# Optimization experiments

Measured on AMD Instinct MI355X. Metric: run time of the kernel, lower is better.

Reference implementation:

```python
import jax, jax.numpy as jnp
import numpy as np

SEQ = 2048
DIM = 512
HEADS = 8
DH = DIM // HEADS
EPS = float(np.finfo(np.float32).eps)
NEG = float(np.finfo(np.float32).max)


def _pos_encoding(seq, dim):
    idx = jnp.arange(seq, dtype=jnp.float32)
    div = 1.0 / (10000.0 ** (jnp.arange(0, dim, 2, dtype=jnp.float32) / dim) + EPS)
    ang = idx[:, None] * div[None, :]  # [S, dim/2]
    pos = jnp.zeros((seq, dim), dtype=jnp.float32)
    pos = pos.at[:, 0::2].set(jnp.sin(ang)).at[:, 1::2].set(jnp.cos(ang))
    return pos[None]  # [1, S, D]


def _rmsnorm(x, gain, bias):
    d = x.shape[-1]
    scale = jnp.linalg.norm(x, axis=-1, keepdims=True) * (d ** -0.5)
    return x / (scale + EPS) * gain + bias


def setup_inputs() -> dict:
    key = jax.random.key(0)
    ks = jax.random.split(key, 12)
    s = 0.02
    return {
        "x": jax.random.normal(ks[0], (4, SEQ, DIM), dtype=jnp.float32),
        "norm1_g": jnp.ones((DIM,), jnp.float32),
        "norm1_b": jnp.zeros((DIM,), jnp.float32),
        "wq": jax.random.normal(ks[1], (DIM, DIM), jnp.float32) * s,
        "wk": jax.random.normal(ks[2], (DIM, DIM), jnp.float32) * s,
        "wv": jax.random.normal(ks[3], (DIM, DIM), jnp.float32) * s,
        "wo": jax.random.normal(ks[4], (DIM, DIM), jnp.float32) * s,
        "norm2_g": jnp.ones((DIM,), jnp.float32),
        "norm2_b": jnp.zeros((DIM,), jnp.float32),
        "ff_w1": jax.random.normal(ks[5], (DIM, DIM), jnp.float32) * s,
        "ff_b1": jnp.zeros((DIM,), jnp.float32),
        "ffn_g": jnp.ones((DIM,), jnp.float32),
        "ffn_b": jnp.zeros((DIM,), jnp.float32),
        "sw_w": jax.random.normal(ks[6], (2 * DIM, DIM), jnp.float32) * s,
        "sw_b": jnp.zeros((2 * DIM,), jnp.float32),
        "ff_w2": jax.random.normal(ks[7], (DIM, DIM), jnp.float32) * s,
        "ff_b2": jnp.zeros((DIM,), jnp.float32),
    }


def _block(x, norm1_g, norm1_b, wq, wk, wv, wo, norm2_g, norm2_b,
           ff_w1, ff_b1, ffn_g, ffn_b, sw_w, sw_b, ff_w2, ff_b2):
    B = x.shape[0]
    x = x + _pos_encoding(SEQ, DIM)

    # --- multi-head attention on RMSNorm(x) ---
    h = _rmsnorm(x, norm1_g, norm1_b)
    q = (h @ wq.T).reshape(B, SEQ, HEADS, DH).transpose(0, 2, 1, 3)  # [B,H,S,Dh]
    k = (h @ wk.T).reshape(B, SEQ, HEADS, DH).transpose(0, 2, 1, 3)
    v = (h @ wv.T).reshape(B, SEQ, HEADS, DH).transpose(0, 2, 1, 3)
    scores = jnp.einsum("bhqd,bhkd->bhqk", q, k)  # materialized [B,H,S,S]
    causal_mask = jnp.triu(jnp.ones((SEQ, SEQ), dtype=bool), k=1)
    scores = jnp.where(causal_mask[None, None], -NEG, scores)
    # NOTE: original scales by dim_k**-0.5 = dim_emb**-0.5 (not head dim)
    attn = jax.nn.softmax(scores * (DIM ** -0.5), axis=-1)
    o = jnp.einsum("bhqk,bhkd->bhqd", attn, v)
    o = o.transpose(0, 2, 1, 3).reshape(B, SEQ, DIM) @ wo.T
    x = x + o

    # --- feed-forward: Linear -> RMSNorm -> SwiGLU -> Linear ---
    h = _rmsnorm(x, norm2_g, norm2_b)
    h = h @ ff_w1.T + ff_b1
    h = _rmsnorm(h, ffn_g, ffn_b)
    u = h @ sw_w.T + sw_b  # [B,S,2*DIM]
    h = jax.nn.silu(u[..., :DIM]) + u[..., DIM:]
    h = h @ ff_w2.T + ff_b2
    return x + h


def reference(x, norm1_g, norm1_b, wq, wk, wv, wo, norm2_g, norm2_b,
              ff_w1, ff_b1, ffn_g, ffn_b, sw_w, sw_b, ff_w2, ff_b2):
    return _block(x, norm1_g, norm1_b, wq, wk, wv, wo, norm2_g, norm2_b,
                  ff_w1, ff_b1, ffn_g, ffn_b, sw_w, sw_b, ff_w2, ff_b2)
```

## Files before the change

### kernel.cpp

```cpp
#include <hip/hip_runtime.h>
#include <hip/hip_bf16.h>
#include <cstdint>
#include <cstddef>

typedef __bf16 bf16;
typedef __bf16 bf16x4_t __attribute__((ext_vector_type(4)));
typedef __bf16 bf16x8_t __attribute__((ext_vector_type(8)));
typedef float f32x4 __attribute__((ext_vector_type(4)));
typedef float f32x16 __attribute__((ext_vector_type(16)));

#define DEV_INLINE __device__ __forceinline__

constexpr int SEQ = 2048, DIM = 512, HEADS = 8, DH = 64;
constexpr int ROWS = 4 * SEQ;
constexpr float EPSF = 1.1920928955078125e-07f;
constexpr float RSQRT_DIM = 0.04419417382415922f;
constexpr float LOG2E = 1.44269504088896f;

DEV_INLINE void load_lds16(const void* g, void* l) {
  __builtin_amdgcn_global_load_lds(
      (const __attribute__((address_space(1))) void*)g,
      (__attribute__((address_space(3))) void*)l,
      16, 0, 0);
}

DEV_INLINE unsigned int packbf(float a, float b) {
  union { unsigned int u; bf16 h[2]; } z;
  z.h[0] = (bf16)a;
  z.h[1] = (bf16)b;
  return z.u;
}

DEV_INLINE void permswap(unsigned int& a, unsigned int& b) {
  asm volatile("v_permlane32_swap_b32 %0, %1" : "+v"(a), "+v"(b));
}

__global__ __launch_bounds__(256) void cvt_all_k(
    const float* __restrict__ wq, const float* __restrict__ wk,
    const float* __restrict__ wv, const float* __restrict__ wo,
    const float* __restrict__ w1, const float* __restrict__ sww,
    const float* __restrict__ w2, bf16* __restrict__ dst) {
  const int i = blockIdx.x * 256 + threadIdx.x;
  const float* src;
  int local;
  if (i < 196608)      { src = (i < 65536) ? wq : (i < 131072) ? wk : wv; local = i & 65535; }
  else if (i < 262144) { src = wo;  local = i - 196608; }
  else if (i < 327680) { src = w1;  local = i - 262144; }
  else if (i < 458752) { src = sww; local = i - 327680; }
  else                 { src = w2;  local = i - 458752; }
  float4 f = reinterpret_cast<const float4*>(src)[local];
  bf16x4_t o;
  o[0] = (bf16)f.x; o[1] = (bf16)f.y; o[2] = (bf16)f.z; o[3] = (bf16)f.w;
  reinterpret_cast<bf16x4_t*>(dst)[i] = o;
}

template <bool ADDPOS>
__global__ __launch_bounds__(256) void rmsnorm_k(const float* __restrict__ in,
                                                 const float* __restrict__ gain,
                                                 const float* __restrict__ bias,
                                                 float* __restrict__ outF,
                                                 bf16* __restrict__ outB) {
  const int sub = threadIdx.x >> 7;
  const int row = blockIdx.x * 2 + sub;
  const int t = threadIdx.x & 127;
  const float* rp = in + (size_t)row * DIM;
  float4 v = reinterpret_cast<const float4*>(rp)[t];
  if constexpr (ADDPOS) {
    const int s = row & (SEQ - 1);
    const float e0 = (float)(4 * t) * (1.0f / (float)DIM);
    const float e1 = (float)(4 * t + 2) * (1.0f / (float)DIM);
    const float d0 = 1.0f / (powf(10000.0f, e0) + EPSF);
    const float d1 = 1.0f / (powf(10000.0f, e1) + EPSF);
    const float a0 = (float)s * d0, a1 = (float)s * d1;
    v.x += sinf(a0); v.y += cosf(a0);
    v.z += sinf(a1); v.w += cosf(a1);
  }
  float ss = v.x * v.x + v.y * v.y + v.z * v.z + v.w * v.w;
#pragma unroll
  for (int off = 32; off > 0; off >>= 1) ss += __shfl_down(ss, off, 64);
  __shared__ float red[4];
  const int wv = threadIdx.x >> 6;
  if ((threadIdx.x & 63) == 0) red[wv] = ss;
  __syncthreads();
  const float total = red[sub * 2] + red[sub * 2 + 1];
  const float scale = sqrtf(total) * RSQRT_DIM;
  const float inv = 1.0f / (scale + EPSF);
  if constexpr (ADDPOS)
    reinterpret_cast<float4*>(outF + (size_t)row * DIM)[t] = v;
  const float4 g = reinterpret_cast<const float4*>(gain)[t];
  const float4 bb = reinterpret_cast<const float4*>(bias)[t];
  bf16x4_t o;
  o[0] = (bf16)(v.x * inv * g.x + bb.x);
  o[1] = (bf16)(v.y * inv * g.y + bb.y);
  o[2] = (bf16)(v.z * inv * g.z + bb.z);
  o[3] = (bf16)(v.w * inv * g.w + bb.w);
  reinterpret_cast<bf16x4_t*>(outB + (size_t)row * DIM)[t] = o;
}

enum { MODE_QKV = 0, MODE_RES = 1, MODE_BIAS = 2, MODE_SWIGLU2 = 3, MODE_RESBIAS = 4 };

template <int MODE>
__global__ __launch_bounds__(256) void gemm_bt_k(
    const bf16* __restrict__ A, const bf16* __restrict__ Bt,
    const float* __restrict__ bias, const float* __restrict__ res,
    float* __restrict__ outF, bf16* __restrict__ outB,
    bf16* __restrict__ oq, bf16* __restrict__ okk, bf16* __restrict__ ovT) {
  constexpr int BELEMS = (MODE == MODE_SWIGLU2) ? 4096 : 2048;
  __shared__ __align__(16) bf16 sA[4][128 * 32];
  __shared__ __align__(16) bf16 sB[4][BELEMS];
  const int tid = threadIdx.x;
  const int wave = tid >> 6, lane = tid & 63;
  const int m0 = blockIdx.x * 128, n0 = blockIdx.y * 64;
  const int wm = wave >> 1, wn = wave & 1;
  const int lr = lane & 15, lk = (lane >> 4) * 8;

  const f32x4 fzero = {0.f, 0.f, 0.f, 0.f};
  f32x4 acc[4][2], acc2[4][2];
#pragma unroll
  for (int i = 0; i < 4; ++i)
#pragma unroll
    for (int j = 0; j < 2; ++j) { acc[i][j] = fzero; acc2[i][j] = fzero; }

  const int off0 = wave * 1024 + lane * 16;
  const int rowS = off0 >> 6, colb = off0 & 63;

  auto stage = [&](int buf, int kt) {
    const int k0 = kt * 32;
    load_lds16((const char*)A + ((size_t)(m0 + rowS) * 512 + k0) * 2 + colb,
               (char*)&sA[buf][0] + off0);
    load_lds16((const char*)A + ((size_t)(m0 + 64 + rowS) * 512 + k0) * 2 + colb,
               (char*)&sA[buf][0] + 4096 + off0);
    load_lds16((const char*)Bt + ((size_t)(n0 + rowS) * 512 + k0) * 2 + colb,
               (char*)&sB[buf][0] + off0);
    if constexpr (MODE == MODE_SWIGLU2)
      load_lds16((const char*)Bt + ((size_t)(512 + n0 + rowS) * 512 + k0) * 2 + colb,
                 (char*)&sB[buf][0] + 4096 + off0);
  };

  stage(0, 0);
  stage(1, 1);
  stage(2, 2);
  if constexpr (MODE == MODE_SWIGLU2)
    asm volatile("s_waitcnt vmcnt(8)\ns_barrier" ::: "memory");
  else
    asm volatile("s_waitcnt vmcnt(6)\ns_barrier" ::: "memory");

#pragma unroll
  for (int kt = 0; kt < 16; ++kt) {
    const int cur = kt & 3;
    if (kt + 3 < 16) stage((kt + 3) & 3, kt + 3);
    bf16x8_t af[4], bfr[2], bfr2[2];
#pragma unroll
    for (int mf = 0; mf < 4; ++mf)
      af[mf] = *(const bf16x8_t*)(&sA[cur][0] + (wm * 64 + mf * 16 + lr) * 32 + lk);
#pragma unroll
    for (int nf = 0; nf < 2; ++nf)
      bfr[nf] = *(const bf16x8_t*)(&sB[cur][0] + (wn * 32 + nf * 16 + lr) * 32 + lk);
    if constexpr (MODE == MODE_SWIGLU2) {
#pragma unroll
      for (int nf = 0; nf < 2; ++nf)
        bfr2[nf] = *(const bf16x8_t*)(&sB[cur][0] + 2048 + (wn * 32 + nf * 16 + lr) * 32 + lk);
    }
    asm volatile("s_waitcnt lgkmcnt(0)" ::: "memory");
#pragma unroll
    for (int mf = 0; mf < 4; ++mf)
#pragma unroll
      for (int nf = 0; nf < 2; ++nf) {
        acc[mf][nf] = __builtin_amdgcn_mfma_f32_16x16x32_bf16(af[mf], bfr[nf],
                                                              acc[mf][nf], 0, 0, 0);
        if constexpr (MODE == MODE_SWIGLU2)
          acc2[mf][nf] = __builtin_amdgcn_mfma_f32_16x16x32_bf16(af[mf], bfr2[nf],
                                                                 acc2[mf][nf], 0, 0, 0);
      }
    if (kt < 13) {
      if constexpr (MODE == MODE_SWIGLU2)
        asm volatile("s_waitcnt vmcnt(8)\ns_barrier" ::: "memory");
      else
        asm volatile("s_waitcnt vmcnt(6)\ns_barrier" ::: "memory");
    } else if (kt == 13) {
      if constexpr (MODE == MODE_SWIGLU2)
        asm volatile("s_waitcnt vmcnt(4)\ns_barrier" ::: "memory");
      else
        asm volatile("s_waitcnt vmcnt(3)\ns_barrier" ::: "memory");
    } else if (kt == 14) {
      asm volatile("s_waitcnt vmcnt(0)\ns_barrier" ::: "memory");
    }
  }

  if constexpr (MODE == MODE_QKV) {
    const int which = n0 >> 9;
    const int h = (n0 >> 6) & 7;
    const int b = m0 >> 11;
    const int s0tok = m0 & 2047;
    bf16* st = &sA[0][0];
    const int rb = wm * 64 + (lane >> 4) * 4;
    const int cb = wn * 32 + lr;
    __syncthreads();
    if (which < 2) {
#pragma unroll
      for (int mf = 0; mf < 4; ++mf)
#pragma unroll
        for (int nf = 0; nf < 2; ++nf)
#pragma unroll
          for (int rg = 0; rg < 4; ++rg) {
            float v = acc[mf][nf][rg];
            if (which == 0) v *= RSQRT_DIM * LOG2E;
            st[(rb + mf * 16 + rg) * 72 + cb + nf * 16] = (bf16)v;
          }
      __syncthreads();
      bf16* dst = which == 0 ? oq : okk;
#pragma unroll
      for (int j = 0; j < 4; ++j) {
        const int flat = j * 4096 + tid * 16;
        const int row = flat >> 7, offb = flat & 127;
        bf16x8_t vv = *(const bf16x8_t*)(st + row * 72 + offb / 2);
        const size_t addr =
            ((size_t)((b * HEADS + h) * SEQ + s0tok + row)) * DH + offb / 2;
        *(bf16x8_t*)(dst + addr) = vv;
      }
    } else {
#pragma unroll
      for (int mf = 0; mf < 4; ++mf)
#pragma unroll
        for (int nf = 0; nf < 2; ++nf)
#pragma unroll
          for (int rg = 0; rg < 4; ++rg)
            st[(cb + nf * 16) * 136 + rb + mf * 16 + rg] = (bf16)acc[mf][nf][rg];
      __syncthreads();
#pragma unroll
      for (int j = 0; j < 4; ++j) {
        const int flat = j * 4096 + tid * 16;
        const int row = flat >> 8, offb = flat & 255;
        bf16x8_t vv = *(const bf16x8_t*)(st + row * 136 + offb / 2);
        const size_t addr =
            ((size_t)((b * HEADS + h) * DH + row)) * SEQ + s0tok + offb / 2;
        *(bf16x8_t*)(ovT + addr) = vv;
      }
    }
    return;
  }

  const int rbase = m0 + wm * 64 + (lane >> 4) * 4;
  const int cbase = n0 + wn * 32 + lr;
#pragma unroll
  for (int mf = 0; mf < 4; ++mf) {
#pragma unroll
    for (int nf = 0; nf < 2; ++nf) {
      const int c = cbase + nf * 16;
#pragma unroll
      for (int rg = 0; rg < 4; ++rg) {
        const int r = rbase + mf * 16 + rg;
        float v = acc[mf][nf][rg];
        if constexpr (MODE == MODE_RES) {
          const size_t idx = (size_t)r * 512 + c;
          outF[idx] = res[idx] + v;
        } else if constexpr (MODE == MODE_BIAS) {
          const size_t idx = (size_t)r * 512 + c;
          outF[idx] = v + bias[c];
        } else if constexpr (MODE == MODE_SWIGLU2) {
          const size_t idx = (size_t)r * 512 + c;
          const float u1 = v + bias[c];
          const float u2 = acc2[mf][nf][rg] + bias[512 + c];
          const float sig = 1.0f / (1.0f + __expf(-u1));
          outB[idx] = (bf16)(u1 * sig + u2);
        } else {
          const size_t idx = (size_t)r * 512 + c;
          outF[idx] = res[idx] + v + bias[c];
        }
      }
    }
  }
}

__constant__ int kSlot[24] = {
  7 | 0,  15 | 16, 15 | 32, 14 | 16, 14 | 32, 6 | 0,  13 | 16, 13 | 32,
  12 | 16, 12 | 32, 5 | 0,  11 | 16, 11 | 32, 10 | 16, 10 | 32, 4 | 0,
  9 | 16, 9 | 32,  8 | 16,  8 | 32,  3 | 0,  2 | 0,  1 | 0,  0 | 0};

__global__ __launch_bounds__(256)
__attribute__((amdgpu_waves_per_eu(2)))
void attn_k(const bf16* __restrict__ Q,
            const bf16* __restrict__ K,
            const bf16* __restrict__ VT,
            bf16* __restrict__ O,
            float* __restrict__ scrO,
            float* __restrict__ scrL) {
  const int tid = threadIdx.x;
  const int wave = tid >> 6, lane = tid & 63;
  const int lq = lane & 31, hi = lane >> 5;

  const int wg = blockIdx.x;
  const int xcd = wg & 7;
  const int bh = xcd * 4 + ((wg >> 3) & 3);
  const int enc = kSlot[wg >> 5];
  const int qi = enc & 15;
  const int mode = enc >> 4;
  const int qw = qi * 128 + wave * 32;
  const int kt0 = (mode == 2) ? (qi + 1) : 0;
  const int ktEnd = (mode == 1) ? (qi + 1) : (2 * qi + 2);
  const int nkt = (mode == 1) ? ktEnd : (2 * qi + 1 + (wave >> 1));

  const char* Kg = (const char*)(K + (size_t)bh * SEQ * DH);
  const char* Vg = (const char*)(VT + (size_t)bh * DH * SEQ);
  const bf16* Qp = Q + (size_t)bh * SEQ * DH;

  __shared__ __align__(16) bf16 smem[6][4096];

  bf16x8_t qf[4];
  {
    const bf16* qp = Qp + (size_t)(qw + lq) * DH + 8 * hi;
    qf[0] = *(const bf16x8_t*)(qp);
    qf[1] = *(const bf16x8_t*)(qp + 16);
    qf[2] = *(const bf16x8_t*)(qp + 32);
    qf[3] = *(const bf16x8_t*)(qp + 48);
  }

  bf16x8_t ones;
#pragma unroll
  for (int i = 0; i < 8; ++i) ones[i] = (bf16)1.0f;

  const int slot = lane & 7, rsub = lane >> 3;
  const int sgoff = (slot * 16) ^ (rsub << 4);

  auto stage = [&](int buf, int kt) {
#pragma unroll
    for (int c = 0; c < 2; ++c) {
      const int row = c * 32 + wave * 8 + rsub;
      const int ldsb = c * 4096 + wave * 1024 + lane * 16;
      load_lds16(Kg + (size_t)(kt * 64 + row) * 128 + sgoff,
                 (char*)&smem[buf][0] + ldsb);
      load_lds16(Vg + (size_t)row * 4096 + (size_t)kt * 128 + sgoff,
                 (char*)&smem[3 + buf][0] + ldsb);
    }
  };

  stage(0, kt0);
  stage(1, kt0 + 1);
  asm volatile("s_waitcnt vmcnt(4)\ns_barrier" ::: "memory");

  f32x16 oa0, oa1, ls;
#pragma unroll
  for (int r = 0; r < 16; ++r) { oa0[r] = 0.f; oa1[r] = 0.f; ls[r] = 0.f; }
  const int xorv = (lq & 7) << 4;

  union U8 { unsigned int u[4]; bf16x8_t v; };

  for (int kt = kt0; kt < ktEnd; ++kt) {
    const int rel = kt - kt0;
    const int buf = rel % 3;
    if (kt + 2 < ktEnd) stage((rel + 2) % 3, kt + 2);
    if (kt < nkt) {
      const char* kb = (const char*)&smem[buf][0];
      const char* vb = (const char*)&smem[3 + buf][0];

      f32x16 s0, s1;
#pragma unroll
      for (int r = 0; r < 16; ++r) { s0[r] = 0.f; s1[r] = 0.f; }
      __builtin_amdgcn_s_setprio(1);
#pragma unroll
      for (int s = 0; s < 4; ++s) {
        const int bo = (32 * s + 16 * hi) ^ xorv;
        s0 = __builtin_amdgcn_mfma_f32_32x32x16_bf16(
            *(const bf16x8_t*)(kb + lq * 128 + bo), qf[s], s0, 0, 0, 0);
        s1 = __builtin_amdgcn_mfma_f32_32x32x16_bf16(
            *(const bf16x8_t*)(kb + (32 + lq) * 128 + bo), qf[s], s1, 0, 0, 0);
      }
      __builtin_amdgcn_s_setprio(0);
      asm volatile("" : "+v"(s0), "+v"(s1));

      if (mode != 1 && kt == nkt - 1) {
        const int qg = qw + lq;
#pragma unroll
        for (int r = 0; r < 16; ++r) {
          const int kl = kt * 64 + (r & 3) + 8 * (r >> 2) + 4 * hi;
          if (kl > qg) s0[r] = -3.0e38f;
          if (kl + 32 > qg) s1[r] = -3.0e38f;
        }
      }

#pragma unroll
      for (int r = 0; r < 16; ++r) {
        s0[r] = exp2f(s0[r]);
        s1[r] = exp2f(s1[r]);
      }

      U8 p00, p01, p10, p11;
      {
        unsigned int x0, x1, y0, y1;
        x0 = packbf(s0[0], s0[1]);  x1 = packbf(s0[4], s0[5]);
        y0 = packbf(s0[2], s0[3]);  y1 = packbf(s0[6], s0[7]);
        permswap(x0, x1); permswap(y0, y1);
        p00.u[0] = x0; p00.u[2] = x1; p00.u[1] = y0; p00.u[3] = y1;
        x0 = packbf(s0[8], s0[9]);   x1 = packbf(s0[12], s0[13]);
        y0 = packbf(s0[10], s0[11]); y1 = packbf(s0[14], s0[15]);
        permswap(x0, x1); permswap(y0, y1);
        p01.u[0] = x0; p01.u[2] = x1; p01.u[1] = y0; p01.u[3] = y1;
        x0 = packbf(s1[0], s1[1]);  x1 = packbf(s1[4], s1[5]);
        y0 = packbf(s1[2], s1[3]);  y1 = packbf(s1[6], s1[7]);
        permswap(x0, x1); permswap(y0, y1);
        p10.u[0] = x0; p10.u[2] = x1; p10.u[1] = y0; p10.u[3] = y1;
        x0 = packbf(s1[8], s1[9]);   x1 = packbf(s1[12], s1[13]);
        y0 = packbf(s1[10], s1[11]); y1 = packbf(s1[14], s1[15]);
        permswap(x0, x1); permswap(y0, y1);
        p11.u[0] = x0; p11.u[2] = x1; p11.u[1] = y0; p11.u[3] = y1;
      }

      ls = __builtin_amdgcn_mfma_f32_32x32x16_bf16(ones, p00.v, ls, 0, 0, 0);
      ls = __builtin_amdgcn_mfma_f32_32x32x16_bf16(ones, p01.v, ls, 0, 0, 0);
      ls = __builtin_amdgcn_mfma_f32_32x32x16_bf16(ones, p10.v, ls, 0, 0, 0);
      ls = __builtin_amdgcn_mfma_f32_32x32x16_bf16(ones, p11.v, ls, 0, 0, 0);

      __builtin_amdgcn_s_setprio(1);
      {
        const int b0 = (16 * hi) ^ xorv;
        const int b1 = (32 + 16 * hi) ^ xorv;
        const int b2 = (64 + 16 * hi) ^ xorv;
        const int b3 = (96 + 16 * hi) ^ xorv;
        oa0 = __builtin_amdgcn_mfma_f32_32x32x16_bf16(
            *(const bf16x8_t*)(vb + lq * 128 + b0), p00.v, oa0, 0, 0, 0);
        oa0 = __builtin_amdgcn_mfma_f32_32x32x16_bf16(
            *(const bf16x8_t*)(vb + lq * 128 + b1), p01.v, oa0, 0, 0, 0);
        oa0 = __builtin_amdgcn_mfma_f32_32x32x16_bf16(
            *(const bf16x8_t*)(vb + lq * 128 + b2), p10.v, oa0, 0, 0, 0);
        oa0 = __builtin_amdgcn_mfma_f32_32x32x16_bf16(
            *(const bf16x8_t*)(vb + lq * 128 + b3), p11.v, oa0, 0, 0, 0);
        oa1 = __builtin_amdgcn_mfma_f32_32x32x16_bf16(
            *(const bf16x8_t*)(vb + (32 + lq) * 128 + b0), p00.v, oa1, 0, 0, 0);
        oa1 = __builtin_amdgcn_mfma_f32_32x32x16_bf16(
            *(const bf16x8_t*)(vb + (32 + lq) * 128 + b1), p01.v, oa1, 0, 0, 0);
        oa1 = __builtin_amdgcn_mfma_f32_32x32x16_bf16(
            *(const bf16x8_t*)(vb + (32 + lq) * 128 + b2), p10.v, oa1, 0, 0, 0);
        oa1 = __builtin_amdgcn_mfma_f32_32x32x16_bf16(
            *(const bf16x8_t*)(vb + (32 + lq) * 128 + b3), p11.v, oa1, 0, 0, 0);
      }
      __builtin_amdgcn_s_setprio(0);
    }
    if (kt + 2 < ktEnd)
      asm volatile("s_waitcnt vmcnt(4)\ns_barrier" ::: "memory");
    else
      asm volatile("s_waitcnt vmcnt(0)\ns_barrier" ::: "memory");
  }

  if (mode == 0) {
    const float inv = 1.0f / ls[0];
    bf16* ol = &smem[0][0] + wave * 2560;
#pragma unroll
    for (int t4 = 0; t4 < 4; ++t4) {
      const int d0 = 8 * t4 + 4 * hi;
      *(unsigned int*)(ol + lq * 80 + d0)          = packbf(oa0[4 * t4] * inv, oa0[4 * t4 + 1] * inv);
      *(unsigned int*)(ol + lq * 80 + d0 + 2)      = packbf(oa0[4 * t4 + 2] * inv, oa0[4 * t4 + 3] * inv);
      *(unsigned int*)(ol + lq * 80 + 32 + d0)     = packbf(oa1[4 * t4] * inv, oa1[4 * t4 + 1] * inv);
      *(unsigned int*)(ol + lq * 80 + 32 + d0 + 2) = packbf(oa1[4 * t4 + 2] * inv, oa1[4 * t4 + 3] * inv);
    }
    const int b = bh >> 3, h = bh & 7;
#pragma unroll
    for (int ps = 0; ps < 4; ++ps) {
      const int flat = ps * 1024 + lane * 16;
      const int qr = flat >> 7, off = flat & 127;
      bf16x8_t vv = *(const bf16x8_t*)((const char*)ol + qr * 160 + off);
      *(bf16x8_t*)(O + ((size_t)(b * SEQ + qw + qr)) * DIM + h * 64 + off / 2) = vv;
    }
  } else {
    const float lrow = ls[0];
    float* so = scrO + ((size_t)(mode - 1) * 256 + bh * 8 + (qi - 8)) * 8192;
    const int qoff = (wave * 32 + lq) * 64;
#pragma unroll
    for (int t4 = 0; t4 < 4; ++t4) {
      const int d0 = 8 * t4 + 4 * hi;
      f32x4 w0 = {oa0[4 * t4], oa0[4 * t4 + 1], oa0[4 * t4 + 2], oa0[4 * t4 + 3]};
      f32x4 w1 = {oa1[4 * t4], oa1[4 * t4 + 1], oa1[4 * t4 + 2], oa1[4 * t4 + 3]};
      *(f32x4*)(so + qoff + d0) = w0;
      *(f32x4*)(so + qoff + 32 + d0) = w1;
    }
    if (!hi)
      scrL[(mode - 1) * 32768 + bh * 1024 + (qi - 8) * 128 + wave * 32 + lq] = lrow;
  }
}

__global__ __launch_bounds__(256) void attn_merge_k(
    const float* __restrict__ scrO, const float* __restrict__ scrL,
    bf16* __restrict__ O) {
  const int i = blockIdx.x * 256 + threadIdx.x;
  const int bh = i >> 14;
  const int rem = i & 16383;
  const int u = rem >> 4;
  const int dq = (rem & 15) << 2;
  const size_t oA = ((size_t)bh * 8 + (u >> 7)) * 8192 + (u & 127) * 64 + dq;
  const f32x4 a = *(const f32x4*)(scrO + oA);
  const f32x4 b = *(const f32x4*)(scrO + 2097152 + oA);
  const float l = scrL[bh * 1024 + u] + scrL[32768 + bh * 1024 + u];
  const float inv = 1.0f / l;
  const int bb = bh >> 3, h = bh & 7;
  bf16x4_t o;
  o[0] = (bf16)((a[0] + b[0]) * inv);
  o[1] = (bf16)((a[1] + b[1]) * inv);
  o[2] = (bf16)((a[2] + b[2]) * inv);
  o[3] = (bf16)((a[3] + b[3]) * inv);
  *(bf16x4_t*)(O + ((size_t)(bb * SEQ + 1024 + u)) * DIM + h * 64 + dq) = o;
}

extern "C" void kernel_launch(void* const* d_in, const int* in_sizes, int n_in,
                              void* d_out, int out_size, void* d_ws, size_t ws_size,
                              hipStream_t stream) {
  const float* x   = (const float*)d_in[0];
  const float* n1g = (const float*)d_in[1];
  const float* n1b = (const float*)d_in[2];
  const float* wq  = (const float*)d_in[3];
  const float* wk  = (const float*)d_in[4];
  const float* wv  = (const float*)d_in[5];
  const float* wo  = (const float*)d_in[6];
  const float* n2g = (const float*)d_in[7];
  const float* n2b = (const float*)d_in[8];
  const float* w1  = (const float*)d_in[9];
  const float* b1  = (const float*)d_in[10];
  const float* ffg = (const float*)d_in[11];
  const float* ffb = (const float*)d_in[12];
  const float* sww = (const float*)d_in[13];
  const float* swb = (const float*)d_in[14];
  const float* w2  = (const float*)d_in[15];
  const float* b2  = (const float*)d_in[16];
  float* out = (float*)d_out;

  char* ws = (char*)d_ws;
  float* x1 = (float*)(ws + 0);
  float* x2 = (float*)(ws + 16777216);
  bf16* hbuf   = (bf16*)(ws + 33554432);
  bf16* qbuf   = (bf16*)(ws + 41943040);
  bf16* kbuf   = (bf16*)(ws + 50331648);
  bf16* vtbuf  = (bf16*)(ws + 58720256);
  bf16* obuf   = (bf16*)(ws + 67108864);
  bf16* wbase  = (bf16*)(ws + 75497472);
  bf16* wqkv_b = wbase;
  bf16* wo_b   = wbase + 786432;
  bf16* w1_b   = wbase + 1048576;
  bf16* sw_b16 = wbase + 1310720;
  bf16* w2_b   = wbase + 1835008;
  float* scrO  = (float*)x2;
  float* scrL  = (float*)hbuf;

  cvt_all_k<<<2048, 256, 0, stream>>>(wq, wk, wv, wo, w1, sww, w2, wbase);

  rmsnorm_k<true><<<ROWS / 2, 256, 0, stream>>>(x, n1g, n1b, x1, hbuf);

  gemm_bt_k<MODE_QKV><<<dim3(64, 24), 256, 0, stream>>>(
      hbuf, wqkv_b, nullptr, nullptr, nullptr, nullptr, qbuf, kbuf, vtbuf);

  attn_k<<<768, 256, 0, stream>>>(qbuf, kbuf, vtbuf, obuf, scrO, scrL);
  attn_merge_k<<<2048, 256, 0, stream>>>(scrO, scrL, obuf);

  gemm_bt_k<MODE_RES><<<dim3(64, 8), 256, 0, stream>>>(
      obuf, wo_b, nullptr, x1, x2, nullptr, nullptr, nullptr, nullptr);

  rmsnorm_k<false><<<ROWS / 2, 256, 0, stream>>>(x2, n2g, n2b, nullptr, hbuf);

  gemm_bt_k<MODE_BIAS><<<dim3(64, 8), 256, 0, stream>>>(
      hbuf, w1_b, b1, nullptr, x1, nullptr, nullptr, nullptr, nullptr);

  rmsnorm_k<false><<<ROWS / 2, 256, 0, stream>>>(x1, ffg, ffb, nullptr, hbuf);

  gemm_bt_k<MODE_SWIGLU2><<<dim3(64, 8), 256, 0, stream>>>(
      hbuf, sw_b16, swb, nullptr, nullptr, qbuf, nullptr, nullptr, nullptr);

  gemm_bt_k<MODE_RESBIAS><<<dim3(64, 8), 256, 0, stream>>>(
      qbuf, w2_b, b2, x2, out, nullptr, nullptr, nullptr, nullptr);
}
```

Before: 158.9 us.

## Double GEMM K-tile depth to 64 with XOR-swizzled LDS layout

The GEMM mainloop now stages K-tiles of 64 instead of 32, which halves the number of barriers and pipeline iterations. Pipeline depth drops to 3 stages, or 2 for the SwiGLU variant, to fit shared memory. Rows are XOR-swizzled in 16-byte chunks on load and read back with a matching swizzle to avoid LDS bank conflicts. The trade-off is more LDS per block, which may lower occupancy, and shallower prefetch that hides less load latency.

Result: faster. 149.5 us (-5.9%).

```diff
diff --git a/kernel.cpp b/kernel.cpp
--- a/kernel.cpp
+++ b/kernel.cpp
@@ -105,14 +105,16 @@
     const float* __restrict__ bias, const float* __restrict__ res,
     float* __restrict__ outF, bf16* __restrict__ outB,
     bf16* __restrict__ oq, bf16* __restrict__ okk, bf16* __restrict__ ovT) {
-  constexpr int BELEMS = (MODE == MODE_SWIGLU2) ? 4096 : 2048;
-  __shared__ __align__(16) bf16 sA[4][128 * 32];
-  __shared__ __align__(16) bf16 sB[4][BELEMS];
+  constexpr int NST = (MODE == MODE_SWIGLU2) ? 2 : 3;
+  constexpr int BELEMS = (MODE == MODE_SWIGLU2) ? 8192 : 4096;
+  __shared__ __align__(16) bf16 sA[NST][128 * 64];
+  __shared__ __align__(16) bf16 sB[NST][BELEMS];
   const int tid = threadIdx.x;
   const int wave = tid >> 6, lane = tid & 63;
   const int m0 = blockIdx.x * 128, n0 = blockIdx.y * 64;
   const int wm = wave >> 1, wn = wave & 1;
-  const int lr = lane & 15, lk = (lane >> 4) * 8;
+  const int lr = lane & 15, hi4 = lane >> 4;
+  const int xw = lr & 7;
 
   const f32x4 fzero = {0.f, 0.f, 0.f, 0.f};
   f32x4 acc[4][2], acc2[4][2];
@@ -121,69 +123,84 @@
 #pragma unroll
     for (int j = 0; j < 2; ++j) { acc[i][j] = fzero; acc2[i][j] = fzero; }
 
-  const int off0 = wave * 1024 + lane * 16;
-  const int rowS = off0 >> 6, colb = off0 & 63;
+  const int rowt = tid >> 3, slot = tid & 7;
+  const int sxor = (slot ^ (rowt & 7)) << 4;
 
   auto stage = [&](int buf, int kt) {
-    const int k0 = kt * 32;
-    load_lds16((const char*)A + ((size_t)(m0 + rowS) * 512 + k0) * 2 + colb,
-               (char*)&sA[buf][0] + off0);
-    load_lds16((const char*)A + ((size_t)(m0 + 64 + rowS) * 512 + k0) * 2 + colb,
-               (char*)&sA[buf][0] + 4096 + off0);
-    load_lds16((const char*)Bt + ((size_t)(n0 + rowS) * 512 + k0) * 2 + colb,
-               (char*)&sB[buf][0] + off0);
-    if constexpr (MODE == MODE_SWIGLU2)
-      load_lds16((const char*)Bt + ((size_t)(512 + n0 + rowS) * 512 + k0) * 2 + colb,
-                 (char*)&sB[buf][0] + 4096 + off0);
+    const size_t k0b = (size_t)kt * 128;
+#pragma unroll
+    for (int c = 0; c < 4; ++c) {
+      const int row = c * 32 + rowt;
+      load_lds16((const char*)A + (size_t)(m0 + row) * 1024 + k0b + sxor,
+                 (char*)&sA[buf][0] + c * 4096 + tid * 16);
+    }
+#pragma unroll
+    for (int c = 0; c < 2; ++c) {
+      const int row = c * 32 + rowt;
+      load_lds16((const char*)Bt + (size_t)(n0 + row) * 1024 + k0b + sxor,
+                 (char*)&sB[buf][0] + c * 4096 + tid * 16);
+    }
+    if constexpr (MODE == MODE_SWIGLU2) {
+#pragma unroll
+      for (int c = 0; c < 2; ++c) {
+        const int row = c * 32 + rowt;
+        load_lds16((const char*)Bt + (size_t)(512 + n0 + row) * 1024 + k0b + sxor,
+                   (char*)&sB[buf][0] + 8192 + c * 4096 + tid * 16);
+      }
+    }
   };
 
-  stage(0, 0);
-  stage(1, 1);
-  stage(2, 2);
-  if constexpr (MODE == MODE_SWIGLU2)
-    asm volatile("s_waitcnt vmcnt(8)\ns_barrier" ::: "memory");
-  else
+  if constexpr (NST == 3) {
+    stage(0, 0);
+    stage(1, 1);
     asm volatile("s_waitcnt vmcnt(6)\ns_barrier" ::: "memory");
-
-#pragma unroll
-  for (int kt = 0; kt < 16; ++kt) {
-    const int cur = kt & 3;
-    if (kt + 3 < 16) stage((kt + 3) & 3, kt + 3);
-    bf16x8_t af[4], bfr[2], bfr2[2];
-#pragma unroll
-    for (int mf = 0; mf < 4; ++mf)
-      af[mf] = *(const bf16x8_t*)(&sA[cur][0] + (wm * 64 + mf * 16 + lr) * 32 + lk);
-#pragma unroll
-    for (int nf = 0; nf < 2; ++nf)
-      bfr[nf] = *(const bf16x8_t*)(&sB[cur][0] + (wn * 32 + nf * 16 + lr) * 32 + lk);
-    if constexpr (MODE == MODE_SWIGLU2) {
-#pragma unroll
-      for (int nf = 0; nf < 2; ++nf)
-        bfr2[nf] = *(const bf16x8_t*)(&sB[cur][0] + 2048 + (wn * 32 + nf * 16 + lr) * 32 + lk);
-    }
-    asm volatile("s_waitcnt lgkmcnt(0)" ::: "memory");
-#pragma unroll
-    for (int mf = 0; mf < 4; ++mf)
+  } else {
+    stage(0, 0);
+    asm volatile("s_waitcnt vmcnt(0)\ns_barrier" ::: "memory");
+  }
+
+#pragma unroll
+  for (int kt = 0; kt < 8; ++kt) {
+    const int cur = kt % NST;
+    if constexpr (NST == 3) {
+      if (kt + 2 < 8) stage((kt + 2) % 3, kt + 2);
+    } else {
+      if (kt + 1 < 8) stage((kt + 1) & 1, kt + 1);
+    }
+    const char* sa = (const char*)&sA[cur][0];
+    const char* sb = (const char*)&sB[cur][0];
+#pragma unroll
+    for (int ks = 0; ks < 2; ++ks) {
+      const int so = ((ks * 4 + hi4) ^ xw) << 4;
+      bf16x8_t af[4], bfr[2], bfr2[2];
+#pragma unroll
+      for (int mf = 0; mf < 4; ++mf)
+        af[mf] = *(const bf16x8_t*)(sa + (wm * 64 + mf * 16 + lr) * 128 + so);
 #pragma unroll
       for (int nf = 0; nf < 2; ++nf) {
-        acc[mf][nf] = __builtin_amdgcn_mfma_f32_16x16x32_bf16(af[mf], bfr[nf],
-                                                              acc[mf][nf], 0, 0, 0);
+        bfr[nf] = *(const bf16x8_t*)(sb + (wn * 32 + nf * 16 + lr) * 128 + so);
         if constexpr (MODE == MODE_SWIGLU2)
-          acc2[mf][nf] = __builtin_amdgcn_mfma_f32_16x16x32_bf16(af[mf], bfr2[nf],
-                                                                 acc2[mf][nf], 0, 0, 0);
-      }
-    if (kt < 13) {
-      if constexpr (MODE == MODE_SWIGLU2)
-        asm volatile("s_waitcnt vmcnt(8)\ns_barrier" ::: "memory");
-      else
+          bfr2[nf] = *(const bf16x8_t*)(sb + 8192 + (wn * 32 + nf * 16 + lr) * 128 + so);
+      }
+#pragma unroll
+      for (int mf = 0; mf < 4; ++mf)
+#pragma unroll
+        for (int nf = 0; nf < 2; ++nf) {
+          acc[mf][nf] = __builtin_amdgcn_mfma_f32_16x16x32_bf16(af[mf], bfr[nf],
+                                                                acc[mf][nf], 0, 0, 0);
+          if constexpr (MODE == MODE_SWIGLU2)
+            acc2[mf][nf] = __builtin_amdgcn_mfma_f32_16x16x32_bf16(af[mf], bfr2[nf],
+                                                                   acc2[mf][nf], 0, 0, 0);
+        }
+    }
+    if constexpr (NST == 3) {
+      if (kt + 2 < 8)
         asm volatile("s_waitcnt vmcnt(6)\ns_barrier" ::: "memory");
-    } else if (kt == 13) {
-      if constexpr (MODE == MODE_SWIGLU2)
-        asm volatile("s_waitcnt vmcnt(4)\ns_barrier" ::: "memory");
-      else
-        asm volatile("s_waitcnt vmcnt(3)\ns_barrier" ::: "memory");
-    } else if (kt == 14) {
-      asm volatile("s_waitcnt vmcnt(0)\ns_barrier" ::: "memory");
+      else if (kt + 1 < 8)
+        asm volatile("s_waitcnt vmcnt(0)\ns_barrier" ::: "memory");
+    } else {
+      if (kt + 1 < 8)
+        asm volatile("s_waitcnt vmcnt(0)\ns_barrier" ::: "memory");
     }
   }
 
@@ -193,7 +210,7 @@
     const int b = m0 >> 11;
     const int s0tok = m0 & 2047;
     bf16* st = &sA[0][0];
-    const int rb = wm * 64 + (lane >> 4) * 4;
+    const int rb = wm * 64 + hi4 * 4;
     const int cb = wn * 32 + lr;
     __syncthreads();
     if (which < 2) {
@@ -240,7 +257,7 @@
     return;
   }
 
-  const int rbase = m0 + wm * 64 + (lane >> 4) * 4;
+  const int rbase = m0 + wm * 64 + hi4 * 4;
   const int cbase = n0 + wn * 32 + lr;
 #pragma unroll
   for (int mf = 0; mf < 4; ++mf) {
```
